# Optimization experiments

Hardware: AMD Instinct MI355X
Metric: run time of the kernel (lower is better)

Reference implementation:

```python
import jax, jax.numpy as jnp
import numpy as np

BN_EPS = 1e-5
NUM_SUBSET = 3


def conv1x1(x, w, b):
    # x: [N, C, T, V], w: [O, C], b: [O]  (1x1 Conv2d)
    return jnp.einsum('nctv,oc->notv', x, w) + b[:, None, None]


def setup_inputs() -> dict:
    key = jax.random.key(0)
    ks = jax.random.split(key, 8)
    N, C, T, V = 64, 64, 300, 25
    IC = 16  # inter_c = out_channels // coff_embedding
    O = 64
    inp = {
        'x': jax.random.normal(ks[0], (N, C, T, V), dtype=jnp.float32),
        'A': jax.random.uniform(ks[1], (NUM_SUBSET, V, V), dtype=jnp.float32),
        'graph_attn': jnp.ones((NUM_SUBSET, V, V), dtype=jnp.float32),
        'g_w': jax.random.normal(ks[2], (NUM_SUBSET, O, C), dtype=jnp.float32) * 0.05,
        'g_b': jnp.zeros((NUM_SUBSET, O), dtype=jnp.float32),
        'a_w': jax.random.normal(ks[3], (NUM_SUBSET, IC, C), dtype=jnp.float32) * 0.05,
        'a_b': jnp.zeros((NUM_SUBSET, IC), dtype=jnp.float32),
        'b_w': jax.random.normal(ks[4], (NUM_SUBSET, IC, C), dtype=jnp.float32) * 0.05,
        'b_b': jnp.zeros((NUM_SUBSET, IC), dtype=jnp.float32),
        'bn_gamma': jnp.ones((O,), dtype=jnp.float32),
        'bn_beta': jnp.zeros((O,), dtype=jnp.float32),
        'bn_mean': jnp.zeros((O,), dtype=jnp.float32),
        'bn_var': jnp.ones((O,), dtype=jnp.float32),
    }
    return inp


def reference(x, A, graph_attn, g_w, g_b, a_w, a_b, b_w, b_b,
              bn_gamma, bn_beta, bn_mean, bn_var):
    N, C, T, V = x.shape
    IC = a_w.shape[1]
    A_tot = A + graph_attn  # [3, V, V]
    x_flat = x.reshape(N, C * T, V)
    hidden = None
    for i in range(NUM_SUBSET):
        # a_conv -> permute(0,3,1,2) -> [N, V, IC*T]
        A1 = conv1x1(x, a_w[i], a_b[i]).transpose(0, 3, 1, 2).reshape(N, V, IC * T)
        # b_conv -> [N, IC*T, V]
        A2 = conv1x1(x, b_w[i], b_b[i]).reshape(N, IC * T, V)
        attn = jax.nn.softmax(jnp.matmul(A1, A2) / (IC * T), axis=-2)  # [N, V, V], softmax over rows
        attn = attn + A_tot[i]
        z = jnp.matmul(x_flat, attn).reshape(N, C, T, V)
        z = conv1x1(z, g_w[i], g_b[i])
        hidden = z if hidden is None else hidden + z
    # BatchNorm2d in eval mode over channel dim
    inv = jax.lax.rsqrt(bn_var + BN_EPS)
    hidden = (hidden - bn_mean[:, None, None]) * (inv * bn_gamma)[:, None, None] + bn_beta[:, None, None]
    # in_channels == out_channels -> identity residual
    hidden = hidden + x
    return jax.nn.relu(hidden)
```

## Files before the change

kernel.cpp:

```cpp
#include <hip/hip_runtime.h>


#define NB 64
#define CB 64
#define TB 300
#define VB 25

typedef unsigned int uint32;
typedef unsigned short ushort16;
typedef __attribute__((ext_vector_type(8))) short short8;
typedef __attribute__((ext_vector_type(4))) float f32x4;
typedef __attribute__((ext_vector_type(16))) float f32x16;

__device__ __forceinline__ ushort16 f2bf(float f) {
    uint32 u = __float_as_uint(f);
    u = u + 0x7FFFu + ((u >> 16) & 1u);
    return (ushort16)(u >> 16);
}
__device__ __forceinline__ float bf2f(ushort16 h) {
    return __uint_as_float(((uint32)h) << 16);
}
__device__ __forceinline__ uint32 packbf2(float a, float b) {
    return (uint32)f2bf(a) | ((uint32)f2bf(b) << 16);
}

__global__ __launch_bounds__(256) void k1_attn_logits_mfma(
    const float* __restrict__ x, const float* __restrict__ a_w,
    const float* __restrict__ a_b, const float* __restrict__ b_w,
    const float* __restrict__ b_b, float* __restrict__ Mb)
{
    __shared__ ushort16 ws[96 * 64];
    __shared__ ushort16 xT[112 * 64];
    __shared__ ushort16 abT[192 * 64];
    __shared__ float    bias[96];

    const int tid   = threadIdx.x;
    const int n     = blockIdx.x / 25;
    const int chunk = blockIdx.x % 25;
    const float* xn = x + n * (CB * TB * VB);

    for (int idx = tid; idx < 6144; idx += 256) {
        int r = idx >> 6, c = idx & 63;
        float v = (r < 48) ? a_w[r * 64 + c] : b_w[(r - 48) * 64 + c];
        ws[r * 64 + ((((c >> 3) + r) & 7) << 3) + (c & 7)] = f2bf(v);
    }
    for (int idx = tid; idx < 96; idx += 256)
        bias[idx] = (idx < 48) ? a_b[idx] : b_b[idx - 48];

    const int w    = tid >> 6;
    const int lane = tid & 63;
    const int l15  = lane & 15;
    const int q    = lane >> 4;
    const int hi   = lane >> 5;
    const int v32  = lane & 31;

    f32x16 acc[3];
    #pragma unroll
    for (int i = 0; i < 3; ++i)
        #pragma unroll
        for (int r = 0; r < 16; ++r) acc[i][r] = 0.f;
    const f32x4 zf = (f32x4){0.f, 0.f, 0.f, 0.f};

    for (int s = 0; s < 3; ++s) {
        __syncthreads();
        const float* xs0 = xn + (chunk * 12 + s * 4) * 25;
        for (int idx = tid; idx < 1600; idx += 256) {
            int c = idx / 25, j = idx % 25;
            float4 v4 = *(const float4*)(xs0 + c * 7500 + j * 4);
            int tv0 = j * 4;
            #pragma unroll
            for (int e = 0; e < 4; ++e) {
                int tv = tv0 + e;
                float fv = (e == 0) ? v4.x : (e == 1) ? v4.y : (e == 2) ? v4.z : v4.w;
                xT[tv * 64 + ((((c >> 3) + tv) & 7) << 3) + (c & 7)] = f2bf(fv);
            }
        }
        __syncthreads();
        for (int tile = w; tile < 42; tile += 4) {
            int rt = tile / 7, ct = tile % 7;
            int r  = rt * 16 + l15;
            int tv = ct * 16 + l15;
            f32x4 d = zf;
            #pragma unroll
            for (int ss = 0; ss < 2; ++ss) {
                int kb = ss * 4 + q;
                short8 af = *(const short8*)&ws[r * 64 + (((kb + r) & 7) << 3)];
                short8 bf = *(const short8*)&xT[tv * 64 + (((kb + tv) & 7) << 3)];
                d = __builtin_amdgcn_mfma_f32_16x16x32_bf16(af, bf, d, 0, 0, 0);
            }
            if (tv < 100) {
                int tl = tv / 25, v = tv % 25;
                int r0 = rt * 16 + q * 4;
                float b0 = bias[r0], b1 = bias[r0 + 1];
                float b2 = bias[r0 + 2], b3 = bias[r0 + 3];
                int kb = tl * 2 + (q >> 1);
                uint32* dst = (uint32*)&abT[(rt * 32 + v) * 64 +
                                            (((kb + v) & 7) << 3) + ((q & 1) << 2)];
                dst[0] = packbf2(d[0] + b0, d[1] + b1);
                dst[1] = packbf2(d[2] + b2, d[3] + b3);
            }
        }
        __syncthreads();
        {
            int kb = w * 2 + hi;
            #pragma unroll
            for (int i = 0; i < 3; ++i) {
                short8 af = *(const short8*)&abT[(i * 32 + v32) * 64 +
                                                 (((kb + v32) & 7) << 3)];
                short8 bf = *(const short8*)&abT[((3 + i) * 32 + v32) * 64 +
                                                 (((kb + v32) & 7) << 3)];
                acc[i] = __builtin_amdgcn_mfma_f32_32x32x16_bf16(af, bf, acc[i], 0, 0, 0);
            }
        }
    }

    float* Ms = (float*)xT;
    __syncthreads();
    for (int idx = tid; idx < 3 * 32 * 33; idx += 256) Ms[idx] = 0.f;
    __syncthreads();
    for (int wv = 0; wv < 4; ++wv) {
        if (w == wv) {
            #pragma unroll
            for (int i = 0; i < 3; ++i)
                #pragma unroll
                for (int r = 0; r < 16; ++r) {
                    int row = (r & 3) + 8 * (r >> 2) + 4 * hi;
                    Ms[i * 1056 + row * 33 + v32] += acc[i][r];
                }
        }
        __syncthreads();
    }
    const float inv = 1.0f / 4800.0f;
    for (int idx = tid; idx < 1875; idx += 256) {
        int i = idx / 625, rem = idx % 625;
        int v1 = rem / 25, v2 = rem % 25;
        atomicAdd(Mb + ((i * NB + n) * 25 + v1) * 25 + v2,
                  Ms[i * 1056 + v1 * 33 + v2] * inv);
    }
}

__global__ __launch_bounds__(256) void k2_softmax_prep(
    const float* __restrict__ Mb, const float* __restrict__ A,
    const float* __restrict__ GA, const float* __restrict__ g_w,
    uint32* __restrict__ atT, uint32* __restrict__ gwb)
{
    int idx = blockIdx.x * 256 + threadIdx.x;
    if (idx < 4800) {
        int v2 = idx % 25, n = (idx / 25) % 64, i = idx / 1600;
        const float* mcol = Mb + ((i * 64 + n) * 25) * 25 + v2;
        float e[25], mx = -1e30f;
        #pragma unroll
        for (int v1 = 0; v1 < 25; ++v1) { e[v1] = mcol[v1 * 25]; mx = fmaxf(mx, e[v1]); }
        float s = 0.f;
        #pragma unroll
        for (int v1 = 0; v1 < 25; ++v1) { e[v1] = __expf(e[v1] - mx); s += e[v1]; }
        float invs = 1.0f / s;
        const float* acol = A + i * 625 + v2;
        const float* gcol = GA + i * 625 + v2;
        float w[25];
        #pragma unroll
        for (int v1 = 0; v1 < 25; ++v1)
            w[v1] = e[v1] * invs + acol[v1 * 25] + gcol[v1 * 25];
        uint32* row = atT + ((i * 64 + n) * 32 + v2) * 16;
        #pragma unroll
        for (int p = 0; p < 12; ++p) row[p] = packbf2(w[2 * p], w[2 * p + 1]);
        row[12] = (uint32)f2bf(w[24]);
        row[13] = 0u; row[14] = 0u; row[15] = 0u;
    } else if (idx < 4800 + 6144) {
        int j = idx - 4800;
        int o = j / 96, kp = j % 96;
        int k0 = 2 * kp;
        int i = k0 >> 6, c = k0 & 63;
        float lo = g_w[(i * 64 + o) * 64 + c];
        float hi = g_w[(i * 64 + o) * 64 + c + 1];
        gwb[o * 96 + kp] = packbf2(lo, hi);
    }
}

__global__ __launch_bounds__(256) void k3_out(
    const float* __restrict__ x, const uint32* __restrict__ atT,
    const ushort16* __restrict__ gwb, const float* __restrict__ g_b,
    const float* __restrict__ bn_g, const float* __restrict__ bn_b,
    const float* __restrict__ bn_m, const float* __restrict__ bn_v,
    float* __restrict__ out)
{
    __shared__ ushort16 xs[64 * 168];
    __shared__ uint32  xa[128 * 36];
    __shared__ uint32  ats[3 * 32 * 20];
    __shared__ float   bsc[64], bsh[64];

    const int tid = threadIdx.x;
    const int n  = blockIdx.x / 60;
    const int t0 = (blockIdx.x % 60) * 5;

    for (int idx = tid; idx < 8000; idx += 256) {
        int c = idx / 125, tv = idx % 125;
        int t = tv / 25, v = tv % 25;
        float g = x[((n * 64 + c) * 300 + t0 + t) * 25 + v];
        xs[c * 168 + t * 32 + v] = f2bf(g);
    }
    for (int idx = tid; idx < 64 * 35; idx += 256) {
        int c = idx / 35, r = idx % 35;
        xs[c * 168 + (r / 7) * 32 + 25 + (r % 7)] = (ushort16)0;
    }
    for (int idx = tid; idx < 1536; idx += 256) {
        int row = idx >> 4, d = idx & 15;
        ats[row * 20 + d] = atT[((row >> 5) * 64 + n) * 512 + (row & 31) * 16 + d];
    }
    for (int idx = tid; idx < 64; idx += 256) {
        float sc = bn_g[idx] * rsqrtf(bn_v[idx] + 1e-5f);
        bsc[idx] = sc;
        bsh[idx] = (g_b[idx] + g_b[64 + idx] + g_b[128 + idx] - bn_m[idx]) * sc + bn_b[idx];
    }
    for (int idx = tid; idx < 3 * 36; idx += 256)
        xa[(125 + idx / 36) * 36 + idx % 36] = 0u;

    const int w    = tid >> 6;
    const int lane = tid & 63;
    const int l15  = lane & 15;
    const int q    = lane >> 4;

    short8 gf[6];
    #pragma unroll
    for (int s = 0; s < 6; ++s)
        gf[s] = *(const short8*)(gwb + ((w * 16 + l15) * 192 + s * 32 + q * 8));

    f32x4 acc[8];
    #pragma unroll
    for (int ct = 0; ct < 8; ++ct) acc[ct] = (f32x4){0.f, 0.f, 0.f, 0.f};
    const f32x4 zf = (f32x4){0.f, 0.f, 0.f, 0.f};

    __syncthreads();

    for (int i = 0; i < 3; ++i) {
        if (i) __syncthreads();
        #pragma unroll
        for (int t = 0; t < 5; ++t) {
            short8 ax = *(const short8*)(xs + (w * 16 + l15) * 168 + t * 32 + q * 8);
            #pragma unroll
            for (int vt = 0; vt < 2; ++vt) {
                short8 bt = *(const short8*)((const ushort16*)ats +
                                             (i * 32 + vt * 16 + l15) * 40 + q * 8);
                f32x4 d = __builtin_amdgcn_mfma_f32_16x16x32_bf16(ax, bt, zf, 0, 0, 0);
                int v2 = vt * 16 + l15;
                if (v2 < 25) {
                    int col = t * 25 + v2;
                    int c0  = w * 16 + q * 4;
                    xa[col * 36 + (c0 >> 1)]     = packbf2(d[0], d[1]);
                    xa[col * 36 + (c0 >> 1) + 1] = packbf2(d[2], d[3]);
                }
            }
        }
        __syncthreads();
        #pragma unroll
        for (int ct = 0; ct < 8; ++ct) {
            #pragma unroll
            for (int s = 0; s < 2; ++s) {
                short8 bfrag = *(const short8*)((const ushort16*)xa +
                                                (ct * 16 + l15) * 72 + s * 32 + q * 8);
                acc[ct] = __builtin_amdgcn_mfma_f32_16x16x32_bf16(
                    gf[i * 2 + s], bfrag, acc[ct], 0, 0, 0);
            }
        }
    }

    const int o0 = w * 16 + q * 4;
    #pragma unroll
    for (int ct = 0; ct < 8; ++ct) {
        int col = ct * 16 + l15;
        if (col < 125) {
            int tl = col / 25;
            int v  = col - tl * 25;
            float* ob = out + (n * 64 + o0) * 7500 + t0 * 25 + col;
            #pragma unroll
            for (int r = 0; r < 4; ++r) {
                int o = o0 + r;
                float xv = bf2f(xs[o * 168 + tl * 32 + v]);
                float h = acc[ct][r] * bsc[o] + bsh[o] + xv;
                ob[r * 7500] = fmaxf(h, 0.f);
            }
        }
    }
}

extern "C" void kernel_launch(void* const* d_in, const int* in_sizes, int n_in,
                              void* d_out, int out_size, void* d_ws, size_t ws_size,
                              hipStream_t stream) {
    const float* x    = (const float*)d_in[0];
    const float* A    = (const float*)d_in[1];
    const float* GA   = (const float*)d_in[2];
    const float* g_w  = (const float*)d_in[3];
    const float* g_b  = (const float*)d_in[4];
    const float* a_w  = (const float*)d_in[5];
    const float* a_b  = (const float*)d_in[6];
    const float* b_w  = (const float*)d_in[7];
    const float* b_b  = (const float*)d_in[8];
    const float* bn_g = (const float*)d_in[9];
    const float* bn_b = (const float*)d_in[10];
    const float* bn_m = (const float*)d_in[11];
    const float* bn_v = (const float*)d_in[12];
    float* out = (float*)d_out;

    float*  Mb  = (float*)d_ws;
    uint32* atT = (uint32*)((char*)d_ws + 480000);
    uint32* gwb = (uint32*)((char*)d_ws + 480000 + 393216);

    hipMemsetAsync(d_ws, 0, 480000, stream);
    k1_attn_logits_mfma<<<dim3(1600), dim3(256), 0, stream>>>(x, a_w, a_b, b_w, b_b, Mb);
    k2_softmax_prep<<<dim3(43), dim3(256), 0, stream>>>(Mb, A, GA, g_w, atT, gwb);
    k3_out<<<dim3(3840), dim3(256), 0, stream>>>(x, atT, (const ushort16*)gwb,
                                                 g_b, bn_g, bn_b, bn_m, bn_v, out);
}
```

Baseline: 371.1 us.

## Prepack conv weights into MFMA fragments and stage whole x slab once

A new tiny kernel pre-packs the a/b conv weights into bf16 MFMA operand fragments, which each k1 wave then loads straight into registers instead of converting and swizzling weights in shared memory per block. k1 now loads its full 300-element x slab once with vectorized bf16 packing and reuses each B fragment across all six row tiles, removing per-substep barriers and repeated tile loads. k3's x staging switches to packed 32-bit bf16 writes with the padding folded in. The cost is an extra launch, higher register pressure from 12 held weight fragments, and strided 16-bit LDS gathers when building B fragments. wpk reuses the atT workspace region, which k2 overwrites afterwards.

```diff
diff --git a/kernel.cpp b/kernel.cpp
--- a/kernel.cpp
+++ b/kernel.cpp
@@ -11,6 +11,7 @@
 typedef __attribute__((ext_vector_type(8))) short short8;
 typedef __attribute__((ext_vector_type(4))) float f32x4;
 typedef __attribute__((ext_vector_type(16))) float f32x16;
+typedef __attribute__((ext_vector_type(4))) uint32 u32x4;
 
 __device__ __forceinline__ ushort16 f2bf(float f) {
     uint32 u = __float_as_uint(f);
@@ -24,25 +25,41 @@
     return (uint32)f2bf(a) | ((uint32)f2bf(b) << 16);
 }
 
+__global__ __launch_bounds__(256) void k0_pack_w(
+    const float* __restrict__ a_w, const float* __restrict__ b_w,
+    uint32* __restrict__ wpk)
+{
+    int idx = blockIdx.x * 256 + threadIdx.x;
+    if (idx < 3072) {
+        int s12 = idx >> 8, rem = idx & 255;
+        int lane = rem >> 2, p = rem & 3;
+        int r = (s12 >> 1) * 16 + (lane & 15);
+        int c = (s12 & 1) * 32 + (lane >> 4) * 8 + 2 * p;
+        const float* row = (r < 48) ? (a_w + r * 64) : (b_w + (r - 48) * 64);
+        wpk[idx] = packbf2(row[c], row[c + 1]);
+    }
+}
+
 __global__ __launch_bounds__(256) void k1_attn_logits_mfma(
-    const float* __restrict__ x, const float* __restrict__ a_w,
-    const float* __restrict__ a_b, const float* __restrict__ b_w,
-    const float* __restrict__ b_b, float* __restrict__ Mb)
+    const float* __restrict__ x, const uint32* __restrict__ wpk,
+    const float* __restrict__ a_b, const float* __restrict__ b_b,
+    float* __restrict__ Mb)
 {
-    __shared__ ushort16 ws[96 * 64];
-    __shared__ ushort16 xT[112 * 64];
+    __shared__ ushort16 slab[64 * 306];
     __shared__ ushort16 abT[192 * 64];
-    __shared__ float    bias[96];
+    __shared__ __align__(16) float bias[96];
 
     const int tid   = threadIdx.x;
     const int n     = blockIdx.x / 25;
     const int chunk = blockIdx.x % 25;
-    const float* xn = x + n * (CB * TB * VB);
-
-    for (int idx = tid; idx < 6144; idx += 256) {
-        int r = idx >> 6, c = idx & 63;
-        float v = (r < 48) ? a_w[r * 64 + c] : b_w[(r - 48) * 64 + c];
-        ws[r * 64 + ((((c >> 3) + r) & 7) << 3) + (c & 7)] = f2bf(v);
+    const float* xn = x + n * (CB * TB * VB) + chunk * 300;
+
+    for (int idx = tid; idx < 4800; idx += 256) {
+        int c = idx / 75, g = idx % 75;
+        float4 v4 = *(const float4*)(xn + c * 7500 + g * 4);
+        uint32* d = (uint32*)&slab[c * 306 + g * 4];
+        d[0] = packbf2(v4.x, v4.y);
+        d[1] = packbf2(v4.z, v4.w);
     }
     for (int idx = tid; idx < 96; idx += 256)
         bias[idx] = (idx < 48) ? a_b[idx] : b_b[idx - 48];
@@ -54,6 +71,11 @@
     const int hi   = lane >> 5;
     const int v32  = lane & 31;
 
+    short8 gfW[12];
+    #pragma unroll
+    for (int s12 = 0; s12 < 12; ++s12)
+        gfW[s12] = ((const short8*)wpk)[s12 * 64 + lane];
+
     f32x16 acc[3];
     #pragma unroll
     for (int i = 0; i < 3; ++i)
@@ -61,43 +83,39 @@
         for (int r = 0; r < 16; ++r) acc[i][r] = 0.f;
     const f32x4 zf = (f32x4){0.f, 0.f, 0.f, 0.f};
 
+    __syncthreads();
+
     for (int s = 0; s < 3; ++s) {
-        __syncthreads();
-        const float* xs0 = xn + (chunk * 12 + s * 4) * 25;
-        for (int idx = tid; idx < 1600; idx += 256) {
-            int c = idx / 25, j = idx % 25;
-            float4 v4 = *(const float4*)(xs0 + c * 7500 + j * 4);
-            int tv0 = j * 4;
-            #pragma unroll
-            for (int e = 0; e < 4; ++e) {
-                int tv = tv0 + e;
-                float fv = (e == 0) ? v4.x : (e == 1) ? v4.y : (e == 2) ? v4.z : v4.w;
-                xT[tv * 64 + ((((c >> 3) + tv) & 7) << 3) + (c & 7)] = f2bf(fv);
-            }
-        }
-        __syncthreads();
-        for (int tile = w; tile < 42; tile += 4) {
-            int rt = tile / 7, ct = tile % 7;
-            int r  = rt * 16 + l15;
-            int tv = ct * 16 + l15;
-            f32x4 d = zf;
-            #pragma unroll
-            for (int ss = 0; ss < 2; ++ss) {
-                int kb = ss * 4 + q;
-                short8 af = *(const short8*)&ws[r * 64 + (((kb + r) & 7) << 3)];
-                short8 bf = *(const short8*)&xT[tv * 64 + (((kb + tv) & 7) << 3)];
-                d = __builtin_amdgcn_mfma_f32_16x16x32_bf16(af, bf, d, 0, 0, 0);
-            }
-            if (tv < 100) {
-                int tl = tv / 25, v = tv % 25;
-                int r0 = rt * 16 + q * 4;
-                float b0 = bias[r0], b1 = bias[r0 + 1];
-                float b2 = bias[r0 + 2], b3 = bias[r0 + 3];
-                int kb = tl * 2 + (q >> 1);
-                uint32* dst = (uint32*)&abT[(rt * 32 + v) * 64 +
-                                            (((kb + v) & 7) << 3) + ((q & 1) << 2)];
-                dst[0] = packbf2(d[0] + b0, d[1] + b1);
-                dst[1] = packbf2(d[2] + b2, d[3] + b3);
+        if (s) __syncthreads();
+        for (int ct = w; ct < 7; ct += 4) {
+            int tvL = ct * 16 + l15;
+            int tvc = s * 100 + tvL;
+            if (tvc > 299) tvc = 299;
+            u32x4 b0v, b1v;
+            #pragma unroll
+            for (int p = 0; p < 4; ++p) {
+                int c0 = q * 8 + 2 * p;
+                b0v[p] = (uint32)slab[c0 * 306 + tvc] |
+                         ((uint32)slab[(c0 + 1) * 306 + tvc] << 16);
+                b1v[p] = (uint32)slab[(c0 + 32) * 306 + tvc] |
+                         ((uint32)slab[(c0 + 33) * 306 + tvc] << 16);
+            }
+            short8 bf0 = __builtin_bit_cast(short8, b0v);
+            short8 bf1 = __builtin_bit_cast(short8, b1v);
+            #pragma unroll
+            for (int rt = 0; rt < 6; ++rt) {
+                f32x4 d = zf;
+                d = __builtin_amdgcn_mfma_f32_16x16x32_bf16(gfW[rt * 2], bf0, d, 0, 0, 0);
+                d = __builtin_amdgcn_mfma_f32_16x16x32_bf16(gfW[rt * 2 + 1], bf1, d, 0, 0, 0);
+                if (tvL < 100) {
+                    float4 bi = *(const float4*)&bias[rt * 16 + q * 4];
+                    int tl = tvL / 25, v = tvL % 25;
+                    int kb = tl * 2 + (q >> 1);
+                    uint32* dst = (uint32*)&abT[(rt * 32 + v) * 64 +
+                                                (((kb + v) & 7) << 3) + ((q & 1) << 2)];
+                    dst[0] = packbf2(d[0] + bi.x, d[1] + bi.y);
+                    dst[1] = packbf2(d[2] + bi.z, d[3] + bi.w);
+                }
             }
         }
         __syncthreads();
@@ -114,7 +132,7 @@
         }
     }
 
-    float* Ms = (float*)xT;
+    float* Ms = (float*)slab;
     __syncthreads();
     for (int idx = tid; idx < 3 * 32 * 33; idx += 256) Ms[idx] = 0.f;
     __syncthreads();
@@ -193,15 +211,20 @@
     const int n  = blockIdx.x / 60;
     const int t0 = (blockIdx.x % 60) * 5;
 
-    for (int idx = tid; idx < 8000; idx += 256) {
-        int c = idx / 125, tv = idx % 125;
-        int t = tv / 25, v = tv % 25;
-        float g = x[((n * 64 + c) * 300 + t0 + t) * 25 + v];
-        xs[c * 168 + t * 32 + v] = f2bf(g);
-    }
-    for (int idx = tid; idx < 64 * 35; idx += 256) {
+    for (int idx = tid; idx < 2240; idx += 256) {
         int c = idx / 35, r = idx % 35;
-        xs[c * 168 + (r / 7) * 32 + 25 + (r % 7)] = (ushort16)0;
+        int t = r / 7, g = r % 7;
+        const float* src = x + ((n * 64 + c) * 300 + t0 + t) * 25;
+        uint32* drow = (uint32*)&xs[c * 168 + t * 32];
+        if (g < 6) {
+            float a0 = src[g * 4 + 0], a1 = src[g * 4 + 1];
+            float a2 = src[g * 4 + 2], a3 = src[g * 4 + 3];
+            drow[g * 2]     = packbf2(a0, a1);
+            drow[g * 2 + 1] = packbf2(a2, a3);
+        } else {
+            drow[12] = (uint32)f2bf(src[24]);
+            drow[13] = 0u; drow[14] = 0u; drow[15] = 0u;
+        }
     }
     for (int idx = tid; idx < 1536; idx += 256) {
         int row = idx >> 4, d = idx & 15;
@@ -304,9 +327,11 @@
     float*  Mb  = (float*)d_ws;
     uint32* atT = (uint32*)((char*)d_ws + 480000);
     uint32* gwb = (uint32*)((char*)d_ws + 480000 + 393216);
+    uint32* wpk = atT;
 
     hipMemsetAsync(d_ws, 0, 480000, stream);
-    k1_attn_logits_mfma<<<dim3(1600), dim3(256), 0, stream>>>(x, a_w, a_b, b_w, b_b, Mb);
+    k0_pack_w<<<dim3(12), dim3(256), 0, stream>>>(a_w, b_w, wpk);
+    k1_attn_logits_mfma<<<dim3(1600), dim3(256), 0, stream>>>(x, wpk, a_b, b_b, Mb);
     k2_softmax_prep<<<dim3(43), dim3(256), 0, stream>>>(Mb, A, GA, g_w, atT, gwb);
     k3_out<<<dim3(3840), dim3(256), 0, stream>>>(x, atT, (const ushort16*)gwb,
                                                  g_b, bn_g, bn_b, bn_m, bn_v, out);
```

New measurement: 381.6 us. 1.03x slower.
